# Kernel optimization log

Measured on AMD Instinct MI355X. Metric: run time of the kernel, lower is better.

The kernel has to match this reference:

```python
import jax, jax.numpy as jnp
import numpy as np
import math

D_MODEL, N_HEADS, D_HEAD = 768, 12, 64
INIT_RANGE = 0.02
ROPE_BASE = 10000.0


def _rope_cos_sin(seq_len, d_head, dtype=jnp.float32):
    # theta_j = base^(-2j/d), positions m -> angles [T, d/2]
    inv_freq = 1.0 / (ROPE_BASE ** (jnp.arange(0, d_head, 2, dtype=jnp.float32) / d_head))
    ang = jnp.arange(seq_len, dtype=jnp.float32)[:, None] * inv_freq[None, :]
    return jnp.cos(ang).astype(dtype), jnp.sin(ang).astype(dtype)


def _apply_rope(x, cos, sin):
    # x: [b, t, h, d]; rotate consecutive (even, odd) pairs as complex numbers
    xr, xi = x[..., 0::2], x[..., 1::2]
    c = cos[None, :, None, :]
    s = sin[None, :, None, :]
    out_r = xr * c - xi * s
    out_i = xr * s + xi * c
    return jnp.stack([out_r, out_i], axis=-1).reshape(x.shape)


def setup_inputs() -> dict:
    key = jax.random.key(0)
    ks = jax.random.split(key, 5)
    B, T = 2, 2048
    x = jax.random.normal(ks[0], (B, T, D_MODEL), dtype=jnp.float32)
    W_Q = INIT_RANGE * jax.random.normal(ks[1], (N_HEADS, D_MODEL, D_HEAD), dtype=jnp.float32)
    W_K = INIT_RANGE * jax.random.normal(ks[2], (N_HEADS, D_MODEL, D_HEAD), dtype=jnp.float32)
    W_V = INIT_RANGE * jax.random.normal(ks[3], (N_HEADS, D_MODEL, D_HEAD), dtype=jnp.float32)
    W_O = INIT_RANGE * jax.random.normal(ks[4], (N_HEADS, D_HEAD, D_MODEL), dtype=jnp.float32)
    b_Q = jnp.zeros((N_HEADS, D_HEAD), dtype=jnp.float32)
    b_K = jnp.zeros((N_HEADS, D_HEAD), dtype=jnp.float32)
    b_V = jnp.zeros((N_HEADS, D_HEAD), dtype=jnp.float32)
    b_O = jnp.zeros((D_MODEL,), dtype=jnp.float32)
    return {"normalized_resid_pre": x, "W_Q": W_Q, "b_Q": b_Q, "W_K": W_K, "b_K": b_K,
            "W_V": W_V, "b_V": b_V, "W_O": W_O, "b_O": b_O}


def reference(normalized_resid_pre, W_Q, b_Q, W_K, b_K, W_V, b_V, W_O, b_O):
    x = normalized_resid_pre
    B, T, _ = x.shape
    cos, sin = _rope_cos_sin(T, D_HEAD, x.dtype)
    Q = jnp.einsum('btc,hcd->bthd', x, W_Q) + b_Q
    K = jnp.einsum('btc,hcd->bthd', x, W_K) + b_K
    V = jnp.einsum('btc,hcd->bthd', x, W_V) + b_V
    Q = _apply_rope(Q, cos, sin)
    K = _apply_rope(K, cos, sin)
    scores = jnp.einsum('bqhd,bkhd->bhqk', Q, K) / math.sqrt(D_HEAD)
    # Faithful to source: tril zeros upper triangle, then all exact zeros -> -inf
    tril = jnp.tril(jnp.ones((T, T), dtype=bool))
    z = jnp.where(tril[None, None], scores, 0.0)
    z = jnp.where(z == 0.0, -jnp.inf, z)
    probs = jax.nn.softmax(z, axis=-1)
    o = jnp.einsum('bhqk,bkhd->bqhd', probs, V)
    return jnp.einsum('bqhd,hdm->bqm', o, W_O) + b_O
```

## Files before the change

kernel.cpp:

```cpp
#include <hip/hip_runtime.h>

typedef unsigned short u16;
typedef unsigned int u32;
typedef short bf16x8 __attribute__((ext_vector_type(8)));
typedef float f32x4 __attribute__((ext_vector_type(4)));
typedef float f32x16 __attribute__((ext_vector_type(16)));

#define MFMA(a, b, c) __builtin_amdgcn_mfma_f32_16x16x32_bf16(a, b, c, 0, 0, 0)
#define MFMA32(a, b, c) __builtin_amdgcn_mfma_f32_32x32x16_bf16(a, b, c, 0, 0, 0)

__device__ __forceinline__ u16 f2bf(float f) {
  unsigned int u = __float_as_uint(f);
  u = (u + 0x7FFFu + ((u >> 16) & 1u)) >> 16;
  return (u16)u;
}

#define GLOAD16(gp, lp)                                                        \
  __builtin_amdgcn_global_load_lds(                                            \
      (const __attribute__((address_space(1))) void*)(gp),                     \
      (__attribute__((address_space(3))) void*)(lp), 16, 0, 0)

__global__ __launch_bounds__(256) void prep_all(
    const float* __restrict__ x, const float* __restrict__ WQ,
    const float* __restrict__ WK, const float* __restrict__ WV,
    const float* __restrict__ WO, float* __restrict__ cost, float* __restrict__ sint,
    u16* __restrict__ xb, u16* __restrict__ Wt, u16* __restrict__ WoT) {
  __shared__ float tile[32][33];
  const int bid = blockIdx.x, tid = threadIdx.x;

  if (bid < 256) {
    int idx = bid * 256 + tid;
    int t = idx >> 5, i = idx & 31;
    float invf = expf(-(float)i * 0.28782313662425572f);
    float ang = (float)t * invf;
    cost[idx] = cosf(ang);
    sint[idx] = sinf(ang);
  } else if (bid < 3328) {
    int i = ((bid - 256) * 256 + tid) * 4;
    float4 v = *(const float4*)(x + i);
    ushort4 o = make_ushort4(f2bf(v.x), f2bf(v.y), f2bf(v.z), f2bf(v.w));
    *(ushort4*)(xb + i) = o;
  } else if (bid < 5056) {
    const int pbid = bid - 3328;
    const int z = pbid / 48, rem = pbid - z * 48;
    const int y = rem / 24, xk = rem - y * 24;
    const int qkv = z / 12, h = z - qkv * 12;
    const float* W = (qkv == 0 ? WQ : qkv == 1 ? WK : WV) + (size_t)h * 768 * 64;
    const int k0 = xk * 32, d0 = y * 32;
    const int tx = tid & 31, ty = tid >> 5;
#pragma unroll
    for (int it = 0; it < 4; it++)
      tile[ty + it * 8][tx] = W[(size_t)(k0 + ty + it * 8) * 64 + d0 + tx];
    __syncthreads();
    u16* out = Wt + (size_t)(qkv * 768 + h * 64 + d0) * 768 + k0;
#pragma unroll
    for (int it = 0; it < 4; it++)
      out[(size_t)(ty + it * 8) * 768 + tx] = f2bf(tile[tx][ty + it * 8]);
  } else {
    const int wbid = bid - 5056;
    const int a0 = (wbid % 24) * 32, m0 = (wbid / 24) * 32;
    const int tx = tid & 31, ty = tid >> 5;
#pragma unroll
    for (int it = 0; it < 4; it++)
      tile[ty + it * 8][tx] = WO[(size_t)(a0 + ty + it * 8) * 768 + m0 + tx];
    __syncthreads();
#pragma unroll
    for (int it = 0; it < 4; it++)
      WoT[(size_t)(m0 + ty + it * 8) * 768 + a0 + tx] = f2bf(tile[tx][ty + it * 8]);
  }
}

template <int MODE>
__global__ __launch_bounds__(256) void gemm_bt(
    const u16* __restrict__ A, const u16* __restrict__ Bt, int K, int LDA, int LDB,
    const float* __restrict__ bQ, const float* __restrict__ bK, const float* __restrict__ bV,
    const float* __restrict__ cost, const float* __restrict__ sint,
    u16* __restrict__ Qb, u16* __restrict__ Kb, u16* __restrict__ Vt,
    const float* __restrict__ bO, float* __restrict__ Out) {
  __shared__ u16 As[2][128 * 64];
  __shared__ u16 Bs[2][128 * 64];
  const int tid = threadIdx.x;
  const int w = tid >> 6, l = tid & 63;
  const int lr = l >> 4, lc = l & 15;
  const int wr = w >> 1, wc = w & 1;

  const int id = blockIdx.x;
  const int xcd = id & 7, idx = id >> 3;
  const int m0 = (xcd * 4 + (idx & 3)) * 128;
  const int n0 = (idx >> 2) * 128;

  f32x4 acc[4][4];
#pragma unroll
  for (int mi = 0; mi < 4; mi++)
#pragma unroll
    for (int ni = 0; ni < 4; ni++) acc[mi][ni] = (f32x4){0.f, 0.f, 0.f, 0.f};

  const int srow = w * 8 + (l >> 3);
  const int sg = (l & 7) ^ (l >> 3);
  const u16* ga = A + (size_t)(m0 + srow) * LDA + sg * 8;
  const u16* gb = Bt + (size_t)(n0 + srow) * LDB + sg * 8;

#define GSTAGE(t, bi)                                                       \
  {                                                                         \
    const int kk = (t) * 64;                                                \
    _Pragma("unroll")                                                       \
    for (int i = 0; i < 4; i++) {                                           \
      GLOAD16(ga + (size_t)(i * 32) * LDA + kk, &As[bi][i * 2048 + w * 512]); \
      GLOAD16(gb + (size_t)(i * 32) * LDB + kk, &Bs[bi][i * 2048 + w * 512]); \
    }                                                                       \
  }

  const int nt = K >> 6;
  GSTAGE(0, 0);

  for (int kt = 0; kt < nt; kt++) {
    asm volatile("s_waitcnt vmcnt(0)" ::: "memory");
    __builtin_amdgcn_s_barrier();
    __builtin_amdgcn_sched_barrier(0);
    if (kt + 1 < nt) GSTAGE(kt + 1, (kt + 1) & 1);

    const char* as = (const char*)As[kt & 1];
    const char* bs = (const char*)Bs[kt & 1];
    bf16x8 af[4][2], bfr[4][2];
#pragma unroll
    for (int mi = 0; mi < 4; mi++) {
      const int row = wr * 64 + mi * 16 + lc;
#pragma unroll
      for (int ks = 0; ks < 2; ks++)
        af[mi][ks] = *(const bf16x8*)(as + row * 128 + (((ks * 4 + lr) ^ (lc & 7)) << 4));
    }
#pragma unroll
    for (int ni = 0; ni < 4; ni++) {
      const int row = wc * 64 + ni * 16 + lc;
#pragma unroll
      for (int ks = 0; ks < 2; ks++)
        bfr[ni][ks] = *(const bf16x8*)(bs + row * 128 + (((ks * 4 + lr) ^ (lc & 7)) << 4));
    }
    __builtin_amdgcn_s_setprio(1);
#pragma unroll
    for (int ks = 0; ks < 2; ks++)
#pragma unroll
      for (int mi = 0; mi < 4; mi++)
#pragma unroll
        for (int ni = 0; ni < 4; ni++)
          acc[mi][ni] = MFMA(af[mi][ks], bfr[ni][ks], acc[mi][ni]);
    __builtin_amdgcn_s_setprio(0);
  }
#undef GSTAGE

#pragma unroll
  for (int mi = 0; mi < 4; mi++) {
#pragma unroll
    for (int ni = 0; ni < 4; ni++) {
      const int col = n0 + wc * 64 + ni * 16 + lc;
      const int rowb = m0 + wr * 64 + mi * 16 + lr * 4;
      if (MODE == 0) {
        const int qkv = col / 768;
        const int rem = col - qkv * 768;
        const int h = rem >> 6, d = rem & 63, fi = d >> 1;
        const float bb = (qkv == 0 ? bQ : qkv == 1 ? bK : bV)[rem];
#pragma unroll
        for (int r = 0; r < 4; r++) {
          const int grow = rowb + r;
          const int t = grow & 2047;
          float v = acc[mi][ni][r] + bb;
          float pv = __shfl_xor(v, 1);
          if (qkv < 2) {
            const float c = cost[t * 32 + fi], s = sint[t * 32 + fi];
            float o = (d & 1) ? (pv * s + v * c) : (v * c - pv * s);
            if (qkv == 0) o *= 0.125f;
            (qkv == 0 ? Qb : Kb)[(size_t)grow * 768 + rem] = f2bf(o);
          } else {
            const int bidx = grow >> 11;
            Vt[((size_t)(bidx * 12 + h) * 64 + d) * 2048 + t] = f2bf(v);
          }
        }
      } else {
        const float bb = bO[col];
#pragma unroll
        for (int r = 0; r < 4; r++) {
          const int grow = rowb + r;
          Out[(size_t)grow * 768 + col] = acc[mi][ni][r] + bb;
        }
      }
    }
  }
}

__global__ __launch_bounds__(256, 2) void attn_kernel(
    const u16* __restrict__ Qb, const u16* __restrict__ Kb,
    const u16* __restrict__ Vt, u16* __restrict__ Ob) {
  __shared__ char Kls[4][8192];
  __shared__ char Vls[4][8192];
  char* scratch = (char*)Kls;

  const int id = blockIdx.x + 16 * blockIdx.y;
  const int s_ = id >> 3;
  const int bh = (id & 7) + 8 * (s_ % 3);
  const int xq = s_ / 3;
  const int b = bh / 12, h = bh - b * 12;
  const int tid = threadIdx.x, w = tid >> 6, l = tid & 63;
  const int lq = l & 31, hi = l >> 5;
  const int qhalf = w & 1, grp = w >> 1;

  const u16* kbase = Kb + (size_t)(b * 2048) * 768 + h * 64;
  const u16* vbase = Vt + (size_t)(bh * 64) * 2048;

  const int r8 = l >> 3;
  const int scol8 = (l & 7) ^ r8;
  const u16* ksrc = kbase + (size_t)(w * 16 + r8) * 768 + scol8 * 8;
  const u16* vsrc = vbase + (size_t)(w * 16 + r8) * 2048 + scol8 * 8;

#define STAGE(t, bi)                                                        \
  {                                                                         \
    const size_t ko = (size_t)(t) * 64 * 768;                               \
    const int vo = (t) * 64;                                                \
    GLOAD16(ksrc + ko,            &Kls[bi][w * 2048]);                      \
    GLOAD16(ksrc + ko + 8 * 768,  &Kls[bi][w * 2048 + 1024]);               \
    GLOAD16(vsrc + vo,            &Vls[bi][w * 2048]);                      \
    GLOAD16(vsrc + vo + 8 * 2048, &Vls[bi][w * 2048 + 1024]);               \
  }

  const int fswz = (lq & 7) << 4;

#pragma unroll 1
  for (int half = 0; half < 2; half++) {
    const int qblk = half == 0 ? 31 - xq : xq;
    const int n = qblk + 1;
    const int nsup = (n + 1) >> 1;

    bf16x8 qf[4];
    {
      const u16* qp = Qb + ((size_t)(b * 2048 + qblk * 64 + qhalf * 32 + lq)) * 768 +
                      h * 64 + hi * 8;
#pragma unroll
      for (int c = 0; c < 4; c++) qf[c] = *(const bf16x8*)(qp + c * 16);
    }

    float m_run = -INFINITY, l_run = 0.f;
    f32x16 acc2[2];
    acc2[0] = (f32x16)0.0f;
    acc2[1] = (f32x16)0.0f;

    STAGE(0, 0);
    if (n > 1) STAGE(1, 1);

    for (int p = 0; p < nsup; p++) {
      const int t0 = 2 * p;
      asm volatile("s_waitcnt vmcnt(0)" ::: "memory");
      __builtin_amdgcn_s_barrier();
      __builtin_amdgcn_sched_barrier(0);
      if (t0 + 2 < n) STAGE(t0 + 2, (t0 + 2) & 3);
      if (t0 + 3 < n) STAGE(t0 + 3, (t0 + 3) & 3);

      const int tile = t0 + grp;
      if (tile < n) {
        const int cur = tile & 3;

        f32x16 s2[2];
        s2[0] = (f32x16)0.0f;
        s2[1] = (f32x16)0.0f;
        __builtin_amdgcn_s_setprio(1);
#pragma unroll
        for (int c = 0; c < 4; c++) {
          const int cb = (c * 32 + hi * 16) ^ fswz;
          bf16x8 kf0 = *(const bf16x8*)(&Kls[cur][lq * 128] + cb);
          bf16x8 kf1 = *(const bf16x8*)(&Kls[cur][(32 + lq) * 128] + cb);
          s2[0] = MFMA32(kf0, qf[c], s2[0]);
          s2[1] = MFMA32(kf1, qf[c], s2[1]);
        }
        __builtin_amdgcn_s_setprio(0);

        if (tile == qblk) {
          const int qrel = qhalf * 32 + lq;
#pragma unroll
          for (int kt2 = 0; kt2 < 2; kt2++)
#pragma unroll
            for (int r = 0; r < 16; r++) {
              const int ko = kt2 * 32 + (r & 3) + 8 * (r >> 2) + 4 * hi;
              if (ko > qrel) s2[kt2][r] = -INFINITY;
            }
        }

        float pm = s2[0][0];
#pragma unroll
        for (int r = 1; r < 16; r++) pm = fmaxf(pm, s2[0][r]);
#pragma unroll
        for (int r = 0; r < 16; r++) pm = fmaxf(pm, s2[1][r]);
        pm = fmaxf(pm, __shfl_xor(pm, 32));

        const float mn = fmaxf(m_run, pm);
        const float alpha = __expf(m_run - mn);
        m_run = mn;

        float rs = 0.f;
        u32 pk[2][8];
#pragma unroll
        for (int kt2 = 0; kt2 < 2; kt2++)
#pragma unroll
          for (int j = 0; j < 8; j++) {
            float p0 = __expf(s2[kt2][2 * j] - mn);
            float p1 = __expf(s2[kt2][2 * j + 1] - mn);
            rs += p0 + p1;
            asm("v_cvt_pk_bf16_f32 %0, %1, %2" : "=v"(pk[kt2][j]) : "v"(p0), "v"(p1));
          }
        l_run = l_run * alpha + rs;

        union { u32 u[4]; bf16x8 v; } pf[4];
#pragma unroll
        for (int kq = 0; kq < 4; kq++) {
          const int kt2 = kq >> 1, i0 = 4 * (kq & 1);
          u32 a0 = pk[kt2][i0], b0 = pk[kt2][i0 + 2];
          u32 a1 = pk[kt2][i0 + 1], b1 = pk[kt2][i0 + 3];
          asm("v_permlane32_swap_b32 %0, %1" : "+v"(a0), "+v"(b0));
          asm("v_permlane32_swap_b32 %0, %1" : "+v"(a1), "+v"(b1));
          pf[kq].u[0] = a0; pf[kq].u[1] = a1; pf[kq].u[2] = b0; pf[kq].u[3] = b1;
        }

#pragma unroll
        for (int dh = 0; dh < 2; dh++)
#pragma unroll
          for (int r = 0; r < 16; r++) acc2[dh][r] *= alpha;

        __builtin_amdgcn_s_setprio(1);
#pragma unroll
        for (int dh = 0; dh < 2; dh++) {
          const char* vr = &Vls[cur][(dh * 32 + lq) * 128];
#pragma unroll
          for (int kq = 0; kq < 4; kq++) {
            bf16x8 vf = *(const bf16x8*)(vr + ((kq * 32 + hi * 16) ^ fswz));
            acc2[dh] = MFMA32(vf, pf[kq].v, acc2[dh]);
          }
        }
        __builtin_amdgcn_s_setprio(0);
      }
    }

    asm volatile("s_waitcnt lgkmcnt(0)" ::: "memory");
    __builtin_amdgcn_s_barrier();
    if (grp == 1) {
      float* sc = (float*)scratch + ((size_t)(w - 2) * 64 + l) * 34;
#pragma unroll
      for (int dh = 0; dh < 2; dh++)
#pragma unroll
        for (int r = 0; r < 16; r++) sc[dh * 16 + r] = acc2[dh][r];
      sc[32] = m_run;
      sc[33] = l_run;
    }
    asm volatile("s_waitcnt lgkmcnt(0)" ::: "memory");
    __builtin_amdgcn_s_barrier();
    if (grp == 0) {
      const float* sc = (const float*)scratch + ((size_t)w * 64 + l) * 34;
      const float m1 = sc[32], l1 = sc[33];
      const float M = fmaxf(m_run, m1);
      const float a0 = __expf(m_run - M);
      const float a1 = __expf(m1 - M);
      const float lm = l_run * a0 + l1 * a1;
      const float lt = lm + __shfl_xor(lm, 32);
      const float inv = 1.0f / lt;
      u16* ob = Ob + ((size_t)(b * 2048 + qblk * 64 + qhalf * 32 + lq)) * 768 + h * 64;
#pragma unroll
      for (int dh = 0; dh < 2; dh++)
#pragma unroll
        for (int g = 0; g < 4; g++) {
          ushort4 o4;
          o4.x = f2bf((acc2[dh][4 * g + 0] * a0 + sc[dh * 16 + 4 * g + 0] * a1) * inv);
          o4.y = f2bf((acc2[dh][4 * g + 1] * a0 + sc[dh * 16 + 4 * g + 1] * a1) * inv);
          o4.z = f2bf((acc2[dh][4 * g + 2] * a0 + sc[dh * 16 + 4 * g + 2] * a1) * inv);
          o4.w = f2bf((acc2[dh][4 * g + 3] * a0 + sc[dh * 16 + 4 * g + 3] * a1) * inv);
          *(ushort4*)(ob + dh * 32 + 8 * g + 4 * hi) = o4;
        }
    }
    asm volatile("s_waitcnt lgkmcnt(0)" ::: "memory");
    __builtin_amdgcn_s_barrier();
  }
#undef STAGE
}


extern "C" void kernel_launch(void* const* d_in, const int* in_sizes, int n_in,
                              void* d_out, int out_size, void* d_ws, size_t ws_size,
                              hipStream_t stream) {
  const float* x  = (const float*)d_in[0];
  const float* WQ = (const float*)d_in[1];
  const float* bQ = (const float*)d_in[2];
  const float* WK = (const float*)d_in[3];
  const float* bK = (const float*)d_in[4];
  const float* WV = (const float*)d_in[5];
  const float* bV = (const float*)d_in[6];
  const float* WO = (const float*)d_in[7];
  const float* bO = (const float*)d_in[8];

  char* ws = (char*)d_ws;
  u16* Xb    = (u16*)(ws + 0);
  u16* Wqkv  = (u16*)(ws + 6291456);
  u16* WoT   = (u16*)(ws + 9830400);
  u16* Qb    = (u16*)(ws + 11010048);
  u16* Kb    = (u16*)(ws + 17301504);
  u16* Vt    = (u16*)(ws + 23592960);
  u16* Ob    = (u16*)(ws + 29884416);
  float* cost = (float*)(ws + 36175872);
  float* sint = (float*)(ws + 36438016);

  prep_all<<<5632, 256, 0, stream>>>(x, WQ, WK, WV, WO, cost, sint, Xb, Wqkv, WoT);

  gemm_bt<0><<<576, 256, 0, stream>>>(Xb, Wqkv, 768, 768, 768,
                                      bQ, bK, bV, cost, sint,
                                      Qb, Kb, Vt, nullptr, nullptr);
  attn_kernel<<<dim3(16, 24), 256, 0, stream>>>(Qb, Kb, Vt, Ob);
  gemm_bt<1><<<192, 256, 0, stream>>>(Ob, WoT, 768, 768, 768,
                                      nullptr, nullptr, nullptr, nullptr, nullptr,
                                      nullptr, nullptr, nullptr, bO, (float*)d_out);
}
```

Baseline: 109.4 us.

## Use 256x256 eight-wave tiles with interleaved prefetch for QKV projection GEMM

Splits the templated GEMM into a dedicated QKV kernel and an output-projection kernel. The QKV kernel uses 256x256 tiles with 512 threads and issues next-stage global-to-LDS loads in four slices interleaved with MFMA sub-phases. This aims to raise data reuse per tile and hide load latency. In exchange it launches only 144 blocks, which leaves many compute units idle, and adds extra barriers per k-step.

```diff
diff --git a/kernel.cpp b/kernel.cpp
--- a/kernel.cpp
+++ b/kernel.cpp
@@ -70,12 +70,128 @@
   }
 }
 
-template <int MODE>
-__global__ __launch_bounds__(256) void gemm_bt(
-    const u16* __restrict__ A, const u16* __restrict__ Bt, int K, int LDA, int LDB,
+__global__ __launch_bounds__(512) void gemm_qkv(
+    const u16* __restrict__ A, const u16* __restrict__ Bt,
     const float* __restrict__ bQ, const float* __restrict__ bK, const float* __restrict__ bV,
     const float* __restrict__ cost, const float* __restrict__ sint,
-    u16* __restrict__ Qb, u16* __restrict__ Kb, u16* __restrict__ Vt,
+    u16* __restrict__ Qb, u16* __restrict__ Kb, u16* __restrict__ Vt) {
+  __shared__ u16 As[2][256 * 64];
+  __shared__ u16 Bs[2][256 * 64];
+  const int tid = threadIdx.x;
+  const int w = tid >> 6, l = tid & 63;
+  const int lr = l >> 4, lc = l & 15;
+  const int wr = w >> 2, wc = w & 3;
+
+  const int wg = (blockIdx.x & 7) * 18 + (blockIdx.x >> 3);
+  const int m0 = (wg & 15) * 256;
+  const int n0 = (wg >> 4) * 256;
+
+  f32x4 acc[8][4];
+#pragma unroll
+  for (int mi = 0; mi < 8; mi++)
+#pragma unroll
+    for (int ni = 0; ni < 4; ni++) acc[mi][ni] = (f32x4){0.f, 0.f, 0.f, 0.f};
+
+  const int sg = (l & 7) ^ (l >> 3);
+  const u16* ga = A + (size_t)(m0 + w * 8 + (l >> 3)) * 768 + sg * 8;
+  const u16* gb = Bt + (size_t)(n0 + w * 8 + (l >> 3)) * 768 + sg * 8;
+
+#define GST(t, bi, i)                                                          \
+  {                                                                            \
+    const int kk = (t) * 64;                                                   \
+    GLOAD16(ga + (size_t)((i) * 64) * 768 + kk, &As[bi][((i) * 64 + w * 8) * 64]); \
+    GLOAD16(gb + (size_t)((i) * 64) * 768 + kk, &Bs[bi][((i) * 64 + w * 8) * 64]); \
+  }
+
+  const int nt = 12;
+  GST(0, 0, 0); GST(0, 0, 1); GST(0, 0, 2); GST(0, 0, 3);
+
+  for (int kt = 0; kt < nt; kt++) {
+    const int cur = kt & 1;
+    const char* as = (const char*)As[cur];
+    const char* bs = (const char*)Bs[cur];
+    bf16x8 bfr[4][2];
+
+#pragma unroll
+    for (int q = 0; q < 4; q++) {
+      bf16x8 af[2][2];
+      if (q == 0) {
+        asm volatile("s_waitcnt vmcnt(0)" ::: "memory");
+        if (kt + 1 < nt) GST(kt + 1, cur ^ 1, 0);
+        __builtin_amdgcn_s_barrier();
+#pragma unroll
+        for (int ni = 0; ni < 4; ni++) {
+          const int row = wc * 64 + ni * 16 + lc;
+#pragma unroll
+          for (int ks = 0; ks < 2; ks++)
+            bfr[ni][ks] = *(const bf16x8*)(bs + row * 128 + (((ks * 4 + lr) ^ (lc & 7)) << 4));
+        }
+#pragma unroll
+        for (int j = 0; j < 2; j++) {
+          const int row = wr * 128 + j * 16 + lc;
+#pragma unroll
+          for (int ks = 0; ks < 2; ks++)
+            af[j][ks] = *(const bf16x8*)(as + row * 128 + (((ks * 4 + lr) ^ (lc & 7)) << 4));
+        }
+      } else {
+#pragma unroll
+        for (int j = 0; j < 2; j++) {
+          const int row = wr * 128 + (2 * q + j) * 16 + lc;
+#pragma unroll
+          for (int ks = 0; ks < 2; ks++)
+            af[j][ks] = *(const bf16x8*)(as + row * 128 + (((ks * 4 + lr) ^ (lc & 7)) << 4));
+        }
+        if (kt + 1 < nt) GST(kt + 1, cur ^ 1, q);
+        __builtin_amdgcn_s_barrier();
+      }
+      asm volatile("s_waitcnt lgkmcnt(0)" ::: "memory");
+      __builtin_amdgcn_sched_barrier(0);
+      __builtin_amdgcn_s_setprio(1);
+#pragma unroll
+      for (int ks = 0; ks < 2; ks++)
+#pragma unroll
+        for (int j = 0; j < 2; j++)
+#pragma unroll
+          for (int ni = 0; ni < 4; ni++)
+            acc[2 * q + j][ni] = MFMA(af[j][ks], bfr[ni][ks], acc[2 * q + j][ni]);
+      __builtin_amdgcn_s_setprio(0);
+      __builtin_amdgcn_s_barrier();
+    }
+  }
+#undef GST
+
+#pragma unroll
+  for (int mi = 0; mi < 8; mi++) {
+#pragma unroll
+    for (int ni = 0; ni < 4; ni++) {
+      const int col = n0 + wc * 64 + ni * 16 + lc;
+      const int rowb = m0 + wr * 128 + mi * 16 + lr * 4;
+      const int qkv = col / 768;
+      const int rem = col - qkv * 768;
+      const int h = rem >> 6, d = rem & 63, fi = d >> 1;
+      const float bb = (qkv == 0 ? bQ : qkv == 1 ? bK : bV)[rem];
+#pragma unroll
+      for (int r = 0; r < 4; r++) {
+        const int grow = rowb + r;
+        const int t = grow & 2047;
+        float v = acc[mi][ni][r] + bb;
+        float pv = __shfl_xor(v, 1);
+        if (qkv < 2) {
+          const float c = cost[t * 32 + fi], s = sint[t * 32 + fi];
+          float o = (d & 1) ? (pv * s + v * c) : (v * c - pv * s);
+          if (qkv == 0) o *= 0.125f;
+          (qkv == 0 ? Qb : Kb)[(size_t)grow * 768 + rem] = f2bf(o);
+        } else {
+          const int bidx = grow >> 11;
+          Vt[((size_t)(bidx * 12 + h) * 64 + d) * 2048 + t] = f2bf(v);
+        }
+      }
+    }
+  }
+}
+
+__global__ __launch_bounds__(256) void gemm_out(
+    const u16* __restrict__ A, const u16* __restrict__ Bt,
     const float* __restrict__ bO, float* __restrict__ Out) {
   __shared__ u16 As[2][128 * 64];
   __shared__ u16 Bs[2][128 * 64];
@@ -97,20 +213,20 @@
 
   const int srow = w * 8 + (l >> 3);
   const int sg = (l & 7) ^ (l >> 3);
-  const u16* ga = A + (size_t)(m0 + srow) * LDA + sg * 8;
-  const u16* gb = Bt + (size_t)(n0 + srow) * LDB + sg * 8;
-
-#define GSTAGE(t, bi)                                                       \
-  {                                                                         \
-    const int kk = (t) * 64;                                                \
-    _Pragma("unroll")                                                       \
-    for (int i = 0; i < 4; i++) {                                           \
-      GLOAD16(ga + (size_t)(i * 32) * LDA + kk, &As[bi][i * 2048 + w * 512]); \
-      GLOAD16(gb + (size_t)(i * 32) * LDB + kk, &Bs[bi][i * 2048 + w * 512]); \
-    }                                                                       \
-  }
-
-  const int nt = K >> 6;
+  const u16* ga = A + (size_t)(m0 + srow) * 768 + sg * 8;
+  const u16* gb = Bt + (size_t)(n0 + srow) * 768 + sg * 8;
+
+#define GSTAGE(t, bi)                                                         \
+  {                                                                           \
+    const int kk = (t) * 64;                                                  \
+    _Pragma("unroll")                                                         \
+    for (int i = 0; i < 4; i++) {                                             \
+      GLOAD16(ga + (size_t)(i * 32) * 768 + kk, &As[bi][i * 2048 + w * 512]); \
+      GLOAD16(gb + (size_t)(i * 32) * 768 + kk, &Bs[bi][i * 2048 + w * 512]); \
+    }                                                                         \
+  }
+
+  const int nt = 12;
   GSTAGE(0, 0);
 
   for (int kt = 0; kt < nt; kt++) {
@@ -154,34 +270,11 @@
     for (int ni = 0; ni < 4; ni++) {
       const int col = n0 + wc * 64 + ni * 16 + lc;
       const int rowb = m0 + wr * 64 + mi * 16 + lr * 4;
-      if (MODE == 0) {
-        const int qkv = col / 768;
-        const int rem = col - qkv * 768;
-        const int h = rem >> 6, d = rem & 63, fi = d >> 1;
-        const float bb = (qkv == 0 ? bQ : qkv == 1 ? bK : bV)[rem];
-#pragma unroll
-        for (int r = 0; r < 4; r++) {
-          const int grow = rowb + r;
-          const int t = grow & 2047;
-          float v = acc[mi][ni][r] + bb;
-          float pv = __shfl_xor(v, 1);
-          if (qkv < 2) {
-            const float c = cost[t * 32 + fi], s = sint[t * 32 + fi];
-            float o = (d & 1) ? (pv * s + v * c) : (v * c - pv * s);
-            if (qkv == 0) o *= 0.125f;
-            (qkv == 0 ? Qb : Kb)[(size_t)grow * 768 + rem] = f2bf(o);
-          } else {
-            const int bidx = grow >> 11;
-            Vt[((size_t)(bidx * 12 + h) * 64 + d) * 2048 + t] = f2bf(v);
-          }
-        }
-      } else {
-        const float bb = bO[col];
-#pragma unroll
-        for (int r = 0; r < 4; r++) {
-          const int grow = rowb + r;
-          Out[(size_t)grow * 768 + col] = acc[mi][ni][r] + bb;
-        }
+      const float bb = bO[col];
+#pragma unroll
+      for (int r = 0; r < 4; r++) {
+        const int grow = rowb + r;
+        Out[(size_t)grow * 768 + col] = acc[mi][ni][r] + bb;
       }
     }
   }
@@ -404,11 +497,7 @@
 
   prep_all<<<5632, 256, 0, stream>>>(x, WQ, WK, WV, WO, cost, sint, Xb, Wqkv, WoT);
 
-  gemm_bt<0><<<576, 256, 0, stream>>>(Xb, Wqkv, 768, 768, 768,
-                                      bQ, bK, bV, cost, sint,
-                                      Qb, Kb, Vt, nullptr, nullptr);
+  gemm_qkv<<<144, 512, 0, stream>>>(Xb, Wqkv, bQ, bK, bV, cost, sint, Qb, Kb, Vt);
   attn_kernel<<<dim3(16, 24), 256, 0, stream>>>(Qb, Kb, Vt, Ob);
-  gemm_bt<1><<<192, 256, 0, stream>>>(Ob, WoT, 768, 768, 768,
-                                      nullptr, nullptr, nullptr, nullptr, nullptr,
-                                      nullptr, nullptr, nullptr, bO, (float*)d_out);
+  gemm_out<<<192, 256, 0, stream>>>(Ob, WoT, bO, (float*)d_out);
 }
```

New measurement: 117.8 us. +7.6%, slower.
